# Kernel tuning notes

Measured on AMD Instinct MI355X. Metric: run time of the kernel, lower is better.

## Reference

```python
import jax, jax.numpy as jnp
import numpy as np

EPS = 1e-6
SCAL = 5.0
PARTS = 16
NFEAT = 32
RES = 64


def conv(x, w, b, stride=1):
    y = jax.lax.conv_general_dilated(x, w, (stride, stride), 'SAME',
                                     dimension_numbers=('NCHW', 'OIHW', 'NCHW'))
    return y + b[None, :, None, None]


def spatial_softmax(x):
    b, k, h, w = x.shape
    return jax.nn.softmax(x.reshape(b, k, h * w), axis=-1).reshape(b, k, h, w)


def make_grid(h, w):
    ys = jnp.linspace(-1.0, 1.0, h)
    xs = jnp.linspace(-1.0, 1.0, w)
    gy, gx = jnp.meshgrid(ys, xs, indexing='ij')
    return jnp.stack([gy, gx], axis=-1)  # [h, w, 2]


def e_sigma(x, w1, b1, w2, b2, wp, bp):
    # shared shape/appearance encoder: parts via spatial softmax + residual sum map
    h1 = jax.nn.relu(conv(x, w1, b1, stride=2))   # [B,64,64,64]
    h2 = jax.nn.relu(conv(h1, w2, b2))            # [B,64,64,64]
    parts = spatial_softmax(conv(h2, wp, bp))     # [B,16,64,64]
    return parts, h2


def e_alpha(x, w1, b1, w2, b2):
    h1 = jax.nn.relu(conv(x, w1, b1))
    return conv(h1, w2, b2)                       # [B,32,64,64]


def get_mu_and_prec(parts):
    # soft-argmax mean + 2x2 covariance -> inverse Cholesky factor L_inv
    b, k, h, w = parts.shape
    grid = make_grid(h, w)
    mu = jnp.einsum('bkhw,hwc->bkc', parts, grid)                       # [b,k,2]
    outer = jnp.einsum('hwm,hwn->hwmn', grid, grid)
    cov = jnp.einsum('bkhw,hwmn->bkmn', parts, outer) - jnp.einsum('bkm,bkn->bkmn', mu, mu)
    a = jnp.sqrt(cov[..., 0, 0] + EPS)
    bb = cov[..., 0, 1] / (a + EPS)
    c = jnp.sqrt(jnp.maximum(cov[..., 1, 1] - bb * bb, 0.0) + EPS)
    det = a * c
    z = jnp.zeros_like(a)
    L_inv = SCAL / (det[..., None, None] + EPS) * jnp.stack(
        [jnp.stack([c, z], axis=-1), jnp.stack([-bb, a], axis=-1)], axis=-2)  # [b,k,2,2]
    return mu, L_inv


def feat_mu_to_enc(alpha, mu, L_inv, h, w):
    # render Cauchy-shaped part heatmaps from (mu, L_inv) and paint part features
    grid = make_grid(h, w)
    dist = grid[None, None] - mu[:, :, None, None, :]        # [b,k,h,w,2]
    proj = jnp.einsum('bkhwi,bkij->bkhwj', dist, L_inv)
    heat = 1.0 / (1.0 + jnp.sum(proj * proj, axis=-1))       # [b,k,h,w]
    norm = heat / (jnp.sum(heat, axis=(2, 3), keepdims=True) + EPS)
    fmap = jnp.einsum('bkf,bkhw->bfhw', alpha, norm)         # [b,nf,h,w]
    return jnp.concatenate([heat, fmap], axis=1)             # [b,nk+nf,h,w]


def decoder(enc, w1, b1, w2, b2, w3, b3):
    h1 = jax.nn.relu(conv(enc, w1, b1))                      # [B,64,64,64]
    up = jnp.repeat(jnp.repeat(h1, 2, axis=2), 2, axis=3)    # nearest upsample -> 128
    h2 = jax.nn.relu(conv(up, w2, b2))
    return jax.nn.sigmoid(conv(h2, w3, b3))                  # [B,3,128,128]


def setup_inputs():
    key = jax.random.key(0)
    ks = jax.random.split(key, 16)
    def w(k, shape):
        fan_in = shape[1] * shape[2] * shape[3]
        return (jax.random.normal(k, shape, jnp.float32) / np.sqrt(fan_in)).astype(jnp.float32)
    B = 32
    return {
        'x': jax.random.uniform(ks[0], (B, 3, 128, 128), jnp.float32),
        'x_spatial_transform': jax.random.uniform(ks[1], (B, 3, 128, 128), jnp.float32),
        'x_appearance_transform': jax.random.uniform(ks[2], (B, 3, 128, 128), jnp.float32),
        'coord': jax.random.normal(ks[3], (B, PARTS, 2), jnp.float32) * 0.5,
        'vector': jax.random.normal(ks[4], (B, PARTS, 2), jnp.float32) * 0.1,
        'es_w1': w(ks[5], (RES, 3, 3, 3)), 'es_b1': jnp.zeros((RES,), jnp.float32),
        'es_w2': w(ks[6], (RES, RES, 3, 3)), 'es_b2': jnp.zeros((RES,), jnp.float32),
        'es_wp': w(ks[7], (PARTS, RES, 3, 3)), 'es_bp': jnp.zeros((PARTS,), jnp.float32),
        'ea_w1': w(ks[8], (RES, RES, 3, 3)), 'ea_b1': jnp.zeros((RES,), jnp.float32),
        'ea_w2': w(ks[9], (NFEAT, RES, 3, 3)), 'ea_b2': jnp.zeros((NFEAT,), jnp.float32),
        'd_w1': w(ks[10], (RES, PARTS + NFEAT, 3, 3)), 'd_b1': jnp.zeros((RES,), jnp.float32),
        'd_w2': w(ks[11], (32, RES, 3, 3)), 'd_b2': jnp.zeros((32,), jnp.float32),
        'd_w3': w(ks[12], (3, 32, 3, 3)), 'd_b3': jnp.zeros((3,), jnp.float32),
    }


def reference(x, x_spatial_transform, x_appearance_transform, coord, vector,
              es_w1, es_b1, es_w2, es_b2, es_wp, es_bp,
              ea_w1, ea_b1, ea_w2, ea_b2,
              d_w1, d_b1, d_w2, d_b2, d_w3, d_b3):
    # shape stream (appearance-transformed image -> geometry)
    shape_parts, _ = e_sigma(x_appearance_transform, es_w1, es_b1, es_w2, es_b2, es_wp, es_bp)
    mu, L_inv = get_mu_and_prec(shape_parts)
    # appearance stream (spatially-transformed image -> appearance)
    app_parts, app_sum = e_sigma(x_spatial_transform, es_w1, es_b1, es_w2, es_b2, es_wp, es_bp)
    f_xs = e_alpha(app_sum, ea_w1, ea_b1, ea_w2, ea_b2)
    # local part appearances: gather features under each part map
    alpha = jnp.einsum('bfhw,bkhw->bkf', f_xs, app_parts)
    encoding = feat_mu_to_enc(alpha, mu, L_inv, 64, 64)
    reconstruction = decoder(encoding, d_w1, d_b1, d_w2, d_b2, d_w3, d_b3)
    # composite loss
    mu_a, L_inv_a = get_mu_and_prec(app_parts)
    rec_loss = jnp.mean((x - reconstruction) ** 2)
    equiv_loss = jnp.mean((mu - mu_a) ** 2) + 0.01 * jnp.mean((L_inv - L_inv_a) ** 2)
    transport_loss = jnp.mean((mu_a - (coord + vector)) ** 2)
    loss = rec_loss + equiv_loss + transport_loss
    return reconstruction, loss
```

## Files before the change

kernel.cpp:

```cpp
#include <hip/hip_runtime.h>
#include <hip/hip_bf16.h>

#define EPS 1e-6f
#define SCAL 5.0f

typedef __attribute__((ext_vector_type(8))) short bf8v;
typedef __attribute__((ext_vector_type(4))) float f32x4;

#define OFF_MU     0
#define OFF_LINV   1024
#define OFF_MUA    3072
#define OFF_LINVA  4096
#define OFF_HSUM   6144
#define OFF_ALPHA  6656
#define OFF_REC    23040
#define OFF_R1     32768
#define OFF_R2     (OFF_R1 + 8388608)
#define OFF_R3     (OFF_R2 + 8388608)
#define WS_TOTAL   (OFF_R3 + 16777216)

#define BA_XA   ((size_t)2 * OFF_R3)
#define BA_X2   ((size_t)2 * OFF_R1)
#define OFF_PARTSF OFF_R2
#define OFF_PROBS  (OFF_R2 + 4194304)
#define BA_EA1  ((size_t)2 * OFF_R3)
#define OFF_FXS (OFF_R3 + 4194304)
#define BA_E    ((size_t)2 * OFF_R2)
#define BA_D1   ((size_t)2 * OFF_R1)
#define BA_D2   ((size_t)2 * OFF_R3)

#define WT_ESW1 0
#define WT_ESB1 1728
#define WT_ESB2 1792
#define WT_ESBP 1856
#define WT_EAB1 1872
#define WT_EAB2 1936
#define WT_DB1  1968
#define WT_DB2  2032
#define WT_W3P  2064
#define WT_DB3  2928
#define P_WP2  0
#define P_WPP  36864
#define P_WPA1 46080
#define P_WPA2 82944
#define P_WPD1 101376
#define P_WPD2 138240

__device__ __attribute__((aligned(16))) float g_ws[WS_TOTAL];
__device__ __attribute__((aligned(16))) float g_wt[3072];
__device__ __attribute__((aligned(16))) __hip_bfloat16 g_wp[156672];
__device__ int g_isbf16;

__device__ __forceinline__ float selz(bool c, float v) { return c ? v : 0.f; }
__device__ __forceinline__ float cvtbf(short s) {
    return __uint_as_float(((unsigned int)(unsigned short)s) << 16);
}
__device__ __forceinline__ short f2bf(float f) {
    unsigned u = __float_as_uint(f);
    u += 0x7fff + ((u >> 16) & 1);
    return (short)(u >> 16);
}
__device__ __forceinline__ float ldin(const void* p, size_t i, int bf) {
    return bf ? __bfloat162float(((const __hip_bfloat16*)p)[i])
              : ((const float*)p)[i];
}

__device__ __forceinline__ float block_sum(float v) {
    __shared__ float sb[8];
    for (int off = 32; off; off >>= 1) v += __shfl_down(v, off, 64);
    int lane = threadIdx.x & 63, wid = threadIdx.x >> 6;
    __syncthreads();
    if (lane == 0) sb[wid] = v;
    __syncthreads();
    float r = 0.f;
    for (int i = 0; i < 4; ++i) r += sb[i];
    return r;
}
__device__ __forceinline__ float block_max(float v) {
    __shared__ float sb[8];
    for (int off = 32; off; off >>= 1) v = fmaxf(v, __shfl_down(v, off, 64));
    int lane = threadIdx.x & 63, wid = threadIdx.x >> 6;
    __syncthreads();
    if (lane == 0) sb[wid] = v;
    __syncthreads();
    float r = -1e30f;
    for (int i = 0; i < 4; ++i) r = fmaxf(r, sb[i]);
    return r;
}

__global__ void detect_k(const void* x) {
    const __hip_bfloat16* p = (const __hip_bfloat16*)x;
    int lane = threadIdx.x & 63;
    float v = 0.f;
    for (int i = lane; i < 256; i += 64) {
        float a = fabsf(__bfloat162float(p[i]));
        if (!(a <= 2.0f)) v = 1.f;
    }
    for (int off = 32; off; off >>= 1) v += __shfl_down(v, off, 64);
    if (lane == 0) {
        g_isbf16 = (v == 0.f) ? 1 : 0;
        g_ws[OFF_REC] = 0.f;
    }
}

__global__ void wpack_k(const void* esw1, const void* esb1, const void* esw2, const void* esb2,
                        const void* eswp, const void* esbp, const void* eaw1, const void* eab1,
                        const void* eaw2, const void* eab2, const void* dw1, const void* db1,
                        const void* dw2, const void* db2, const void* dw3, const void* db3) {
    int bf = g_isbf16;
    int gid0 = blockIdx.x * 256 + threadIdx.x, stride = gridDim.x * 256;
    for (int g = gid0; g < 512; g += stride) g_ws[OFF_HSUM + g] = 0.f;
    for (int g = gid0; g < 1728; g += stride) g_wt[WT_ESW1 + g] = ldin(esw1, g, bf);
    for (int g = gid0; g < 64; g += stride) g_wt[WT_ESB1 + g] = ldin(esb1, g, bf);
    for (int g = gid0; g < 64; g += stride) g_wt[WT_ESB2 + g] = ldin(esb2, g, bf);
    for (int g = gid0; g < 16; g += stride) g_wt[WT_ESBP + g] = ldin(esbp, g, bf);
    for (int g = gid0; g < 64; g += stride) g_wt[WT_EAB1 + g] = ldin(eab1, g, bf);
    for (int g = gid0; g < 32; g += stride) g_wt[WT_EAB2 + g] = ldin(eab2, g, bf);
    for (int g = gid0; g < 64; g += stride) g_wt[WT_DB1 + g] = ldin(db1, g, bf);
    for (int g = gid0; g < 32; g += stride) g_wt[WT_DB2 + g] = ldin(db2, g, bf);
    for (int g = gid0; g < 3; g += stride) g_wt[WT_DB3 + g] = ldin(db3, g, bf);
    for (int g = gid0; g < 864; g += stride) {
        int t = g / 96, o = (g / 32) % 3, k = g & 31;
        g_wt[WT_W3P + g] = ldin(dw3, (size_t)(o * 32 + k) * 9 + t, bf);
    }
    for (int g = gid0; g < 36864; g += stride) {
        int t = g >> 12, n = (g >> 6) & 63, k = g & 63;
        g_wp[P_WP2 + g] = __float2bfloat16(ldin(esw2, (size_t)(n * 64 + k) * 9 + t, bf));
    }
    for (int g = gid0; g < 9216; g += stride) {
        int t = g >> 10, n = (g >> 6) & 15, k = g & 63;
        g_wp[P_WPP + g] = __float2bfloat16(ldin(eswp, (size_t)(n * 64 + k) * 9 + t, bf));
    }
    for (int g = gid0; g < 36864; g += stride) {
        int t = g >> 12, n = (g >> 6) & 63, k = g & 63;
        g_wp[P_WPA1 + g] = __float2bfloat16(ldin(eaw1, (size_t)(n * 64 + k) * 9 + t, bf));
    }
    for (int g = gid0; g < 18432; g += stride) {
        int t = g >> 11, n = (g >> 6) & 31, k = g & 63;
        g_wp[P_WPA2 + g] = __float2bfloat16(ldin(eaw2, (size_t)(n * 64 + k) * 9 + t, bf));
    }
    for (int g = gid0; g < 36864; g += stride) {
        int t = g >> 12, n = (g >> 6) & 63, k = g & 63;
        float v = (k < 48) ? ldin(dw1, (size_t)(n * 48 + k) * 9 + t, bf) : 0.f;
        g_wp[P_WPD1 + g] = __float2bfloat16(v);
    }
    for (int g = gid0; g < 18432; g += stride) {
        int t = g >> 11, n = (g >> 6) & 31, k = g & 63;
        g_wp[P_WPD2 + g] = __float2bfloat16(ldin(dw2, (size_t)(n * 64 + k) * 9 + t, bf));
    }
}

__global__ void __launch_bounds__(256)
conv_s2n_k(const void* __restrict__ inA, const void* __restrict__ inB) {
    int bf = g_isbf16;
    int tile = blockIdx.x & 15;
    int gb = blockIdx.x >> 4;
    int g = gb & 3, b = gb >> 2;
    const void* in = (b < 32) ? inA : inB;
    int bb = b & 31;
    int pix = tile * 256 + threadIdx.x;
    int y = pix >> 6, x = pix & 63;
    size_t inb = (size_t)bb * 3 * 16384;
    const float* W = g_wt + WT_ESW1 + (size_t)(g * 16) * 27;
    float acc[16];
    #pragma unroll
    for (int o = 0; o < 16; ++o) acc[o] = g_wt[WT_ESB1 + g * 16 + o];
    int iy0 = 2 * y, ix0 = 2 * x;
    bool my2 = (iy0 + 2 < 128), mx2 = (ix0 + 2 < 128);
    int iy2 = my2 ? iy0 + 2 : 127, ix2 = mx2 ? ix0 + 2 : 127;
    for (int ic = 0; ic < 3; ++ic) {
        size_t pb = inb + ic * 16384;
        float t[9];
        t[0] = ldin(in, pb + iy0 * 128 + ix0, bf);
        t[1] = ldin(in, pb + iy0 * 128 + ix0 + 1, bf);
        t[2] = selz(mx2, ldin(in, pb + iy0 * 128 + ix2, bf));
        t[3] = ldin(in, pb + (iy0 + 1) * 128 + ix0, bf);
        t[4] = ldin(in, pb + (iy0 + 1) * 128 + ix0 + 1, bf);
        t[5] = selz(mx2, ldin(in, pb + (iy0 + 1) * 128 + ix2, bf));
        t[6] = selz(my2, ldin(in, pb + iy2 * 128 + ix0, bf));
        t[7] = selz(my2, ldin(in, pb + iy2 * 128 + ix0 + 1, bf));
        t[8] = selz(my2 && mx2, ldin(in, pb + iy2 * 128 + ix2, bf));
        #pragma unroll
        for (int o = 0; o < 16; ++o) {
            const float* wr = W + (o * 3 + ic) * 9;
            float a = acc[o];
            #pragma unroll
            for (int j = 0; j < 9; ++j) a = fmaf(t[j], wr[j], a);
            acc[o] = a;
        }
    }
    __hip_bfloat16* out = (__hip_bfloat16*)g_ws + BA_XA + ((size_t)b * 4096 + pix) * 64 + g * 16;
    #pragma unroll
    for (int o = 0; o < 16; ++o) out[o] = __float2bfloat16(fmaxf(acc[o], 0.f));
}

template<int TR>
__device__ __forceinline__ void stage_tile(__hip_bfloat16* sA,
                                           const __hip_bfloat16* __restrict__ inb, int y0) {
    for (int g = threadIdx.x; g < TR * 512; g += 256) {
        int r = g >> 9;
        int rem = g & 511;
        int px = rem >> 3, j = rem & 7;
        int yy = y0 - 1 + r;
        int P = px + 1;
        bf8v v = (bf8v){0, 0, 0, 0, 0, 0, 0, 0};
        if (yy >= 0 && yy <= 63)
            v = *(const bf8v*)(inb + ((size_t)(yy * 64 + px) * 64 + j * 8));
        *(bf8v*)(sA + ((r * 66 + P) * 64 + ((j ^ (P & 7)) * 8))) = v;
    }
    if (threadIdx.x < TR * 16) {
        int g = threadIdx.x;
        int r = g >> 4, rem = g & 15, side = rem >> 3, j = rem & 7;
        int P = side ? 65 : 0;
        *(bf8v*)(sA + ((r * 66 + P) * 64 + ((j ^ (P & 7)) * 8))) = (bf8v){0, 0, 0, 0, 0, 0, 0, 0};
    }
}

template<int MS>
__device__ __forceinline__ void ld_a(const __hip_bfloat16* sA, int it, int rowIn,
                                     int l15, int quad, bf8v (&a)[MS]) {
    const int t = it >> 1, c = it & 1;
    const int dy = t / 3 - 1, dx = t % 3 - 1;
    const int r = rowIn + 1 + dy;
    const int j = c * 4 + quad;
    #pragma unroll
    for (int ms = 0; ms < MS; ++ms) {
        int P = ms * 16 + l15 + dx + 1;
        a[ms] = *(const bf8v*)(sA + ((r * 66 + P) * 64 + ((j ^ (P & 7)) * 8)));
    }
}
template<int TOTN, int NS>
__device__ __forceinline__ void ld_b(int it, int l15, int quad, int wp_off, bf8v (&bv)[NS]) {
    const int t = it >> 1, c = it & 1;
    #pragma unroll
    for (int ns = 0; ns < NS; ++ns)
        bv[ns] = *(const bf8v*)(g_wp + wp_off +
                 ((size_t)(t * TOTN + ns * 16 + l15) * 64 + c * 32 + quad * 8));
}

template<int TOTN, int NS, int MS>
__device__ __forceinline__ void conv_body(const __hip_bfloat16* sA, int rowIn,
                                          int l15, int quad, int wp_off,
                                          f32x4 (&acc)[MS][NS]) {
    bf8v bq[3][NS];
    bf8v a[2][MS];
    ld_b<TOTN, NS>(0, l15, quad, wp_off, bq[0]);
    ld_b<TOTN, NS>(1, l15, quad, wp_off, bq[1]);
    ld_a<MS>(sA, 0, rowIn, l15, quad, a[0]);
    #pragma unroll
    for (int it = 0; it < 18; ++it) {
        if (it + 2 < 18) ld_b<TOTN, NS>(it + 2, l15, quad, wp_off, bq[(it + 2) % 3]);
        if (it + 1 < 18) ld_a<MS>(sA, it + 1, rowIn, l15, quad, a[(it + 1) & 1]);
        #pragma unroll
        for (int ns = 0; ns < NS; ++ns)
            #pragma unroll
            for (int ms = 0; ms < MS; ++ms)
                acc[ms][ns] = __builtin_amdgcn_mfma_f32_16x16x32_bf16(
                    a[it & 1][ms], bq[it % 3][ns], acc[ms][ns], 0, 0, 0);
    }
}

template<int TOTN, int NS, int OUTF32, int RELU>
__device__ __forceinline__ void epi_std(f32x4 (&acc)[4][NS], int bO, int y,
                                        int l15, int quad, int bias_off, size_t out_off) {
    #pragma unroll
    for (int ns = 0; ns < NS; ++ns) {
        float bias = g_wt[bias_off + ns * 16 + l15];
        #pragma unroll
        for (int ms = 0; ms < 4; ++ms) {
            #pragma unroll
            for (int r = 0; r < 4; ++r) {
                int pix = ms * 16 + quad * 4 + r;
                float v = acc[ms][ns][r] + bias;
                if (RELU) v = fmaxf(v, 0.f);
                size_t o = out_off + ((size_t)(bO * 4096 + y * 64 + pix)) * TOTN + ns * 16 + l15;
                if (OUTF32) g_ws[o] = v;
                else ((__hip_bfloat16*)g_ws)[o] = __float2bfloat16(v);
            }
        }
    }
}

template<int TOTN, int NS, int OUTF32, int RELU>
__global__ void __launch_bounds__(256) __attribute__((amdgpu_waves_per_eu(2, 3)))
conv_mfl_k(size_t in_off, int wp_off, int bias_off, size_t out_off) {
    __shared__ __hip_bfloat16 sA[6 * 66 * 64];
    int wid = threadIdx.x >> 6, lane = threadIdx.x & 63;
    int l15 = lane & 15, quad = lane >> 4;
    int b = blockIdx.x >> 4, y0 = (blockIdx.x & 15) * 4;
    const __hip_bfloat16* inb = (const __hip_bfloat16*)g_ws + in_off + (size_t)b * 4096 * 64;
    stage_tile<6>(sA, inb, y0);
    __syncthreads();
    f32x4 acc[4][NS];
    #pragma unroll
    for (int ms = 0; ms < 4; ++ms)
        #pragma unroll
        for (int ns = 0; ns < NS; ++ns) acc[ms][ns] = (f32x4){0.f, 0.f, 0.f, 0.f};
    conv_body<TOTN, NS, 4>(sA, wid, l15, quad, wp_off, acc);
    epi_std<TOTN, NS, OUTF32, RELU>(acc, b, y0 + wid, l15, quad, bias_off, out_off);
}

__global__ void __launch_bounds__(256) __attribute__((amdgpu_waves_per_eu(2, 3)))
conv_pea_k() {
    __shared__ __hip_bfloat16 sA[6 * 66 * 64];
    int wid = threadIdx.x >> 6, lane = threadIdx.x & 63;
    int l15 = lane & 15, quad = lane >> 4;
    int b = blockIdx.x >> 4, y0 = (blockIdx.x & 15) * 4;
    int y = y0 + wid;
    const __hip_bfloat16* inb = (const __hip_bfloat16*)g_ws + BA_X2 + (size_t)b * 4096 * 64;
    stage_tile<6>(sA, inb, y0);
    __syncthreads();
    f32x4 accP[4][1];
    #pragma unroll
    for (int ms = 0; ms < 4; ++ms) accP[ms][0] = (f32x4){0.f, 0.f, 0.f, 0.f};
    conv_body<16, 1, 4>(sA, wid, l15, quad, P_WPP, accP);
    epi_std<16, 1, 1, 0>(accP, b, y, l15, quad, WT_ESBP, (size_t)OFF_PARTSF);
    if (b >= 32) {
        f32x4 accE[4][4];
        #pragma unroll
        for (int ms = 0; ms < 4; ++ms)
            #pragma unroll
            for (int ns = 0; ns < 4; ++ns) accE[ms][ns] = (f32x4){0.f, 0.f, 0.f, 0.f};
        conv_body<64, 4, 4>(sA, wid, l15, quad, P_WPA1, accE);
        epi_std<64, 4, 0, 1>(accE, b - 32, y, l15, quad, WT_EAB1, BA_EA1);
    }
}

__global__ void __launch_bounds__(256) __attribute__((amdgpu_waves_per_eu(2, 3)))
conv_upmf2_k(size_t in_off, int wp_off, int bias_off, size_t out_off) {
    __shared__ __hip_bfloat16 sA[4 * 66 * 64];
    int wid = threadIdx.x >> 6, lane = threadIdx.x & 63;
    int l15 = lane & 15, quad = lane >> 4;
    int b = blockIdx.x >> 5, y0 = (blockIdx.x & 31) * 4;
    int ri0 = (y0 >> 1) - 1;
    const __hip_bfloat16* inb = (const __hip_bfloat16*)g_ws + in_off + (size_t)b * 4096 * 64;
    for (int g = threadIdx.x; g < 2048; g += 256) {
        int r = g >> 9;
        int rem = g & 511;
        int px = rem >> 3, j = rem & 7;
        int yi = ri0 + r;
        int P = px + 1;
        bf8v v = (bf8v){0, 0, 0, 0, 0, 0, 0, 0};
        if (yi >= 0 && yi <= 63)
            v = *(const bf8v*)(inb + ((size_t)(yi * 64 + px) * 64 + j * 8));
        *(bf8v*)(sA + ((r * 66 + P) * 64 + ((j ^ (P & 7)) * 8))) = v;
    }
    if (threadIdx.x < 64) {
        int g = threadIdx.x;
        int r = g >> 4, rem = g & 15, side = rem >> 3, j = rem & 7;
        int P = side ? 65 : 0;
        *(bf8v*)(sA + ((r * 66 + P) * 64 + ((j ^ (P & 7)) * 8))) = (bf8v){0, 0, 0, 0, 0, 0, 0, 0};
    }
    __syncthreads();
    int y = y0 + wid;
    f32x4 acc[8][2];
    #pragma unroll
    for (int ms = 0; ms < 8; ++ms)
        #pragma unroll
        for (int ns = 0; ns < 2; ++ns) acc[ms][ns] = (f32x4){0.f, 0.f, 0.f, 0.f};
    bf8v bq[3][2];
    ld_b<32, 2>(0, l15, quad, wp_off, bq[0]);
    ld_b<32, 2>(1, l15, quad, wp_off, bq[1]);
    #pragma unroll
    for (int it = 0; it < 18; ++it) {
        if (it + 2 < 18) ld_b<32, 2>(it + 2, l15, quad, wp_off, bq[(it + 2) % 3]);
        const int t = it >> 1, c = it & 1;
        const int dy = t / 3 - 1, dx = t % 3 - 1;
        int yy = y + dy;
        if (yy >= 0 && yy <= 127) {
            int r = (yy >> 1) - ri0;
            int j = c * 4 + quad;
            bf8v a[8];
            #pragma unroll
            for (int ms = 0; ms < 8; ++ms) {
                int xx = ms * 16 + l15 + dx;
                int P = (xx < 0) ? 0 : ((xx > 127) ? 65 : ((xx >> 1) + 1));
                a[ms] = *(const bf8v*)(sA + ((r * 66 + P) * 64 + ((j ^ (P & 7)) * 8)));
            }
            #pragma unroll
            for (int ns = 0; ns < 2; ++ns)
                #pragma unroll
                for (int ms = 0; ms < 8; ++ms)
                    acc[ms][ns] = __builtin_amdgcn_mfma_f32_16x16x32_bf16(a[ms], bq[it % 3][ns], acc[ms][ns], 0, 0, 0);
        }
    }
    #pragma unroll
    for (int ns = 0; ns < 2; ++ns) {
        float bias = g_wt[bias_off + ns * 16 + l15];
        #pragma unroll
        for (int ms = 0; ms < 8; ++ms) {
            #pragma unroll
            for (int r = 0; r < 4; ++r) {
                int pix = ms * 16 + quad * 4 + r;
                float v = fmaxf(acc[ms][ns][r] + bias, 0.f);
                size_t o = out_off + ((size_t)(b * 16384 + y * 128 + pix)) * 32 + ns * 16 + l15;
                ((__hip_bfloat16*)g_ws)[o] = __float2bfloat16(v);
            }
        }
    }
}

__global__ void sm_mom3_k() {
    int bk = blockIdx.x;
    int b = bk >> 4, k = bk & 15;
    int app = (b >= 32);
    const float* P = g_ws + OFF_PARTSF + (size_t)b * 4096 * 16 + k;
    float r[16];
    #pragma unroll
    for (int j = 0; j < 16; ++j) r[j] = P[(size_t)(threadIdx.x + j * 256) * 16];
    float m = r[0];
    #pragma unroll
    for (int j = 1; j < 16; ++j) m = fmaxf(m, r[j]);
    m = block_max(m);
    float s = 0.f;
    #pragma unroll
    for (int j = 0; j < 16; ++j) { r[j] = __expf(r[j] - m); s += r[j]; }
    s = block_sum(s);
    float inv = 1.0f / s;
    float sy = 0, sx = 0, syy = 0, sxy = 0, sxx = 0;
    #pragma unroll
    for (int j = 0; j < 16; ++j) {
        float pv = r[j] * inv;
        int i = threadIdx.x + j * 256;
        if (app) g_ws[OFF_PROBS + ((size_t)(b - 32) * 16 + k) * 4096 + i] = pv;
        float gy = -1.0f + (i >> 6) * (2.0f / 63.0f);
        float gx = -1.0f + (i & 63) * (2.0f / 63.0f);
        sy += pv * gy; sx += pv * gx;
        syy += pv * gy * gy; sxy += pv * gy * gx; sxx += pv * gx * gx;
    }
    sy = block_sum(sy); sx = block_sum(sx);
    syy = block_sum(syy); sxy = block_sum(sxy); sxx = block_sum(sxx);
    if (threadIdx.x == 0) {
        float c00 = syy - sy * sy, c01 = sxy - sy * sx, c11 = sxx - sx * sx;
        float a = sqrtf(fmaxf(c00 + EPS, 1e-12f));
        float bb = c01 / (a + EPS);
        float cc = sqrtf(fmaxf(c11 - bb * bb, 0.f) + EPS);
        float det = a * cc;
        float sc = SCAL / (det + EPS);
        int idx = app ? ((b - 32) * 16 + k) : (b * 16 + k);
        int mu_off = app ? OFF_MUA : OFF_MU;
        int linv_off = app ? OFF_LINVA : OFF_LINV;
        g_ws[mu_off + idx * 2 + 0] = sy;
        g_ws[mu_off + idx * 2 + 1] = sx;
        g_ws[linv_off + idx * 4 + 0] = cc * sc;
        g_ws[linv_off + idx * 4 + 1] = 0.f;
        g_ws[linv_off + idx * 4 + 2] = -bb * sc;
        g_ws[linv_off + idx * 4 + 3] = a * sc;
    }
}

__global__ void alpha2_k() {
    int b = blockIdx.x & 31, k = blockIdx.x >> 5;
    int bk = b * 16 + k;
    __shared__ float pl[4096];
    const float* pr = g_ws + OFF_PROBS + (size_t)bk * 4096;
    for (int i = threadIdx.x; i < 4096; i += 256) pl[i] = pr[i];
    __syncthreads();
    float acc[32];
    #pragma unroll
    for (int f = 0; f < 32; ++f) acc[f] = 0.f;
    for (int i = threadIdx.x; i < 4096; i += 256) {
        float pv = pl[i];
        const float* fp = g_ws + OFF_FXS + (size_t)(b * 4096 + i) * 32;
        #pragma unroll
        for (int f = 0; f < 32; ++f) acc[f] = fmaf(pv, fp[f], acc[f]);
    }
    __shared__ float sw[4][32];
    int lane = threadIdx.x & 63, wid = threadIdx.x >> 6;
    #pragma unroll
    for (int f = 0; f < 32; ++f)
        for (int off = 32; off; off >>= 1) acc[f] += __shfl_down(acc[f], off, 64);
    if (lane == 0) {
        #pragma unroll
        for (int f = 0; f < 32; ++f) sw[wid][f] = acc[f];
    }
    __syncthreads();
    if (threadIdx.x < 32)
        g_ws[OFF_ALPHA + bk * 32 + threadIdx.x] =
            sw[0][threadIdx.x] + sw[1][threadIdx.x] + sw[2][threadIdx.x] + sw[3][threadIdx.x];
}

__global__ void heat2_k() {
    int tile = blockIdx.x & 15, b = blockIdx.x >> 4;
    __shared__ float hs[16];
    if (threadIdx.x < 16) hs[threadIdx.x] = 0.f;
    __syncthreads();
    int pix = tile * 256 + threadIdx.x;
    float gy = -1.0f + (pix >> 6) * (2.0f / 63.0f);
    float gx = -1.0f + (pix & 63) * (2.0f / 63.0f);
    bf8v e0, e1;
    float hv[16];
    #pragma unroll
    for (int k = 0; k < 16; ++k) {
        int bk = b * 16 + k;
        float m0 = g_ws[OFF_MU + bk * 2], m1 = g_ws[OFF_MU + bk * 2 + 1];
        float L00 = g_ws[OFF_LINV + bk * 4 + 0], L10 = g_ws[OFF_LINV + bk * 4 + 2],
              L11 = g_ws[OFF_LINV + bk * 4 + 3];
        float d0 = gy - m0, d1 = gx - m1;
        float p0 = d0 * L00 + d1 * L10;
        float p1 = d1 * L11;
        float h = 1.0f / (1.0f + p0 * p0 + p1 * p1);
        hv[k] = h;
        short sbits = f2bf(h);
        if (k < 8) e0[k] = sbits; else e1[k - 8] = sbits;
    }
    __hip_bfloat16* E = (__hip_bfloat16*)g_ws + BA_E + (size_t)(b * 4096 + pix) * 64;
    *(bf8v*)E = e0;
    *(bf8v*)(E + 8) = e1;
    #pragma unroll
    for (int k = 0; k < 16; ++k) {
        float v = hv[k];
        for (int off = 32; off; off >>= 1) v += __shfl_down(v, off, 64);
        if ((threadIdx.x & 63) == 0) atomicAdd(&hs[k], v);
    }
    __syncthreads();
    if (threadIdx.x < 16)
        atomicAdd(&g_ws[OFF_HSUM + b * 16 + threadIdx.x], hs[threadIdx.x]);
}

__global__ void fmap2_k() {
    int tile = blockIdx.x & 15, b = blockIdx.x >> 4;
    __shared__ float coef[16][32];
    for (int i = threadIdx.x; i < 512; i += 256) {
        int k = i >> 5, f = i & 31;
        coef[k][f] = g_ws[OFF_ALPHA + (b * 16 + k) * 32 + f] /
                     (g_ws[OFF_HSUM + b * 16 + k] + EPS);
    }
    __syncthreads();
    int pix = tile * 256 + threadIdx.x;
    __hip_bfloat16* E = (__hip_bfloat16*)g_ws + BA_E + (size_t)(b * 4096 + pix) * 64;
    float h[16];
    #pragma unroll
    for (int k = 0; k < 16; ++k) h[k] = __bfloat162float(E[k]);
    #pragma unroll
    for (int f = 0; f < 32; ++f) {
        float a = 0.f;
        #pragma unroll
        for (int k = 0; k < 16; ++k) a = fmaf(h[k], coef[k][f], a);
        E[16 + f] = __float2bfloat16(a);
    }
    #pragma unroll
    for (int z = 48; z < 64; ++z) E[z] = __float2bfloat16(0.f);
}

__global__ void __launch_bounds__(256)
conv_sign_k(const void* __restrict__ ximg, void* __restrict__ outp) {
    int bf = g_isbf16;
    int tile = blockIdx.x & 63, b = blockIdx.x >> 6;
    int pix = tile * 256 + threadIdx.x;
    int y = pix >> 7, x = pix & 127;
    const short* D2 = (const short*)((const __hip_bfloat16*)g_ws + BA_D2 + (size_t)b * 16384 * 32);
    float acc[3];
    #pragma unroll
    for (int o = 0; o < 3; ++o) acc[o] = g_wt[WT_DB3 + o];
    #pragma unroll
    for (int t = 0; t < 9; ++t) {
        int dy = t / 3 - 1, dx = t % 3 - 1;
        int yy = y + dy, xx = x + dx;
        if (yy < 0 || yy > 127 || xx < 0 || xx > 127) continue;
        const short* sp = D2 + (size_t)(yy * 128 + xx) * 32;
        #pragma unroll
        for (int c = 0; c < 4; ++c) {
            bf8v v = *(const bf8v*)(sp + c * 8);
            #pragma unroll
            for (int j = 0; j < 8; ++j) {
                float av = cvtbf(v[j]);
                int k = c * 8 + j;
                acc[0] = fmaf(av, g_wt[WT_W3P + (t * 3 + 0) * 32 + k], acc[0]);
                acc[1] = fmaf(av, g_wt[WT_W3P + (t * 3 + 1) * 32 + k], acc[1]);
                acc[2] = fmaf(av, g_wt[WT_W3P + (t * 3 + 2) * 32 + k], acc[2]);
            }
        }
    }
    float es = 0.f;
    #pragma unroll
    for (int o = 0; o < 3; ++o) {
        float v = 1.0f / (1.0f + __expf(-acc[o]));
        size_t oidx = ((size_t)b * 3 + o) * 16384 + pix;
        if (bf) ((__hip_bfloat16*)outp)[oidx] = __float2bfloat16(v);
        else    ((float*)outp)[oidx] = v;
        float e = ldin(ximg, oidx, bf) - v;
        es += e * e;
    }
    float s = block_sum(es);
    if (threadIdx.x == 0) atomicAdd(&g_ws[OFF_REC], s);
}

__global__ void loss_k(const void* __restrict__ coord,
                       const void* __restrict__ vec,
                       void* __restrict__ outp) {
    int bf = g_isbf16;
    const float* mu = g_ws + OFF_MU;
    const float* linv = g_ws + OFF_LINV;
    const float* mu_a = g_ws + OFF_MUA;
    const float* linv_a = g_ws + OFF_LINVA;
    float s1 = 0, s2 = 0, s3 = 0;
    for (int i = threadIdx.x; i < 1024; i += 256) {
        float d = mu[i] - mu_a[i];
        s1 += d * d;
        float t = ldin(coord, i, bf) + ldin(vec, i, bf);
        float d3 = mu_a[i] - t;
        s3 += d3 * d3;
    }
    for (int i = threadIdx.x; i < 2048; i += 256) {
        float d = linv[i] - linv_a[i];
        s2 += d * d;
    }
    s1 = block_sum(s1);
    s2 = block_sum(s2);
    s3 = block_sum(s3);
    if (threadIdx.x == 0) {
        float loss = g_ws[OFF_REC] / 1572864.0f + s1 / 1024.0f + 0.01f * (s2 / 2048.0f)
                   + s3 / 1024.0f;
        if (bf) ((__hip_bfloat16*)outp)[1572864] = __float2bfloat16(loss);
        else    ((float*)outp)[1572864] = loss;
    }
}

extern "C" void kernel_launch(void* const* d_in, const int* in_sizes, int n_in,
                              void* d_out, int out_size, void* d_ws, size_t ws_size,
                              hipStream_t stream) {
    const void* x     = d_in[0];
    const void* x_st  = d_in[1];
    const void* x_at  = d_in[2];
    const void* coord = d_in[3];
    const void* vec   = d_in[4];

    dim3 blk(256);

    detect_k<<<1, 64, 0, stream>>>(x);
    wpack_k<<<64, blk, 0, stream>>>(
        d_in[5],  d_in[6],  d_in[7],  d_in[8],
        d_in[9],  d_in[10], d_in[11], d_in[12],
        d_in[13], d_in[14], d_in[15], d_in[16],
        d_in[17], d_in[18], d_in[19], d_in[20]);

    conv_s2n_k<<<64 * 4 * 16, blk, 0, stream>>>(x_at, x_st);
    conv_mfl_k<64, 4, 0, 1><<<1024, blk, 0, stream>>>(BA_XA, P_WP2, WT_ESB2, BA_X2);

    conv_pea_k<<<1024, blk, 0, stream>>>();
    sm_mom3_k<<<1024, blk, 0, stream>>>();

    conv_mfl_k<32, 2, 1, 0><<<512, blk, 0, stream>>>(BA_EA1, P_WPA2, WT_EAB2, (size_t)OFF_FXS);
    alpha2_k<<<512, blk, 0, stream>>>();

    heat2_k<<<512, blk, 0, stream>>>();
    fmap2_k<<<512, blk, 0, stream>>>();

    conv_mfl_k<64, 4, 0, 1><<<512, blk, 0, stream>>>(BA_E, P_WPD1, WT_DB1, BA_D1);
    conv_upmf2_k<<<1024, blk, 0, stream>>>(BA_D1, P_WPD2, WT_DB2, BA_D2);
    conv_sign_k<<<32 * 64, blk, 0, stream>>>(x, d_out);

    loss_k<<<1, blk, 0, stream>>>(coord, vec, d_out);
}
```

Baseline: 417.8 us.

## Split conv warp tiles into two rows by half the output channels

Reorganises the warp work split in the MFMA conv kernels. Each of the four waves now computes two output rows for half of the output channels, instead of one row for all channels. Each wave therefore loads only half the weight fragments from global memory, and each weight fragment is reused across two rows. The cost is twice as many shared-memory A-fragment reads per weight set, with a similar accumulator register count.

```diff
diff --git a/kernel.cpp b/kernel.cpp
--- a/kernel.cpp
+++ b/kernel.cpp
@@ -229,13 +229,30 @@
         a[ms] = *(const bf8v*)(sA + ((r * 66 + P) * 64 + ((j ^ (P & 7)) * 8)));
     }
 }
+template<int MS>
+__device__ __forceinline__ void ld_a2(const __hip_bfloat16* sA, int it, int rowbase,
+                                      int l15, int quad, bf8v (&a)[2][MS]) {
+    const int t = it >> 1, c = it & 1;
+    const int dy = t / 3 - 1, dx = t % 3 - 1;
+    const int j = c * 4 + quad;
+    #pragma unroll
+    for (int rp = 0; rp < 2; ++rp) {
+        const int r = rowbase + rp + 1 + dy;
+        #pragma unroll
+        for (int ms = 0; ms < MS; ++ms) {
+            int P = ms * 16 + l15 + dx + 1;
+            a[rp][ms] = *(const bf8v*)(sA + ((r * 66 + P) * 64 + ((j ^ (P & 7)) * 8)));
+        }
+    }
+}
 template<int TOTN, int NS>
-__device__ __forceinline__ void ld_b(int it, int l15, int quad, int wp_off, bf8v (&bv)[NS]) {
+__device__ __forceinline__ void ld_b(int it, int ocoff, int l15, int quad, int wp_off,
+                                     bf8v (&bv)[NS]) {
     const int t = it >> 1, c = it & 1;
     #pragma unroll
     for (int ns = 0; ns < NS; ++ns)
         bv[ns] = *(const bf8v*)(g_wp + wp_off +
-                 ((size_t)(t * TOTN + ns * 16 + l15) * 64 + c * 32 + quad * 8));
+                 ((size_t)(t * TOTN + ocoff + ns * 16 + l15) * 64 + c * 32 + quad * 8));
 }
 
 template<int TOTN, int NS, int MS>
@@ -244,12 +261,12 @@
                                           f32x4 (&acc)[MS][NS]) {
     bf8v bq[3][NS];
     bf8v a[2][MS];
-    ld_b<TOTN, NS>(0, l15, quad, wp_off, bq[0]);
-    ld_b<TOTN, NS>(1, l15, quad, wp_off, bq[1]);
+    ld_b<TOTN, NS>(0, 0, l15, quad, wp_off, bq[0]);
+    ld_b<TOTN, NS>(1, 0, l15, quad, wp_off, bq[1]);
     ld_a<MS>(sA, 0, rowIn, l15, quad, a[0]);
     #pragma unroll
     for (int it = 0; it < 18; ++it) {
-        if (it + 2 < 18) ld_b<TOTN, NS>(it + 2, l15, quad, wp_off, bq[(it + 2) % 3]);
+        if (it + 2 < 18) ld_b<TOTN, NS>(it + 2, 0, l15, quad, wp_off, bq[(it + 2) % 3]);
         if (it + 1 < 18) ld_a<MS>(sA, it + 1, rowIn, l15, quad, a[(it + 1) & 1]);
         #pragma unroll
         for (int ns = 0; ns < NS; ++ns)
@@ -257,6 +274,30 @@
             for (int ms = 0; ms < MS; ++ms)
                 acc[ms][ns] = __builtin_amdgcn_mfma_f32_16x16x32_bf16(
                     a[it & 1][ms], bq[it % 3][ns], acc[ms][ns], 0, 0, 0);
+    }
+}
+
+template<int TOTN, int NSW, int MS>
+__device__ __forceinline__ void conv_body2(const __hip_bfloat16* sA, int rowbase, int ocoff,
+                                           int l15, int quad, int wp_off,
+                                           f32x4 (&acc)[2][MS][NSW]) {
+    bf8v bq[3][NSW];
+    bf8v a[2][2][MS];
+    ld_b<TOTN, NSW>(0, ocoff, l15, quad, wp_off, bq[0]);
+    ld_b<TOTN, NSW>(1, ocoff, l15, quad, wp_off, bq[1]);
+    ld_a2<MS>(sA, 0, rowbase, l15, quad, a[0]);
+    #pragma unroll
+    for (int it = 0; it < 18; ++it) {
+        if (it + 2 < 18) ld_b<TOTN, NSW>(it + 2, ocoff, l15, quad, wp_off, bq[(it + 2) % 3]);
+        if (it + 1 < 18) ld_a2<MS>(sA, it + 1, rowbase, l15, quad, a[(it + 1) & 1]);
+        #pragma unroll
+        for (int rp = 0; rp < 2; ++rp)
+            #pragma unroll
+            for (int ns = 0; ns < NSW; ++ns)
+                #pragma unroll
+                for (int ms = 0; ms < MS; ++ms)
+                    acc[rp][ms][ns] = __builtin_amdgcn_mfma_f32_16x16x32_bf16(
+                        a[it & 1][rp][ms], bq[it % 3][ns], acc[rp][ms][ns], 0, 0, 0);
     }
 }
 
@@ -280,24 +321,54 @@
         }
     }
 }
-
-template<int TOTN, int NS, int OUTF32, int RELU>
+template<int TOTN, int NSW, int OUTF32, int RELU>
+__device__ __forceinline__ void epi_2r(f32x4 (&acc)[2][4][NSW], int bO, int y0, int rowbase,
+                                       int ocoff, int l15, int quad, int bias_off,
+                                       size_t out_off) {
+    #pragma unroll
+    for (int rp = 0; rp < 2; ++rp) {
+        int y = y0 + rowbase + rp;
+        #pragma unroll
+        for (int ns = 0; ns < NSW; ++ns) {
+            float bias = g_wt[bias_off + ocoff + ns * 16 + l15];
+            #pragma unroll
+            for (int ms = 0; ms < 4; ++ms) {
+                #pragma unroll
+                for (int r = 0; r < 4; ++r) {
+                    int pix = ms * 16 + quad * 4 + r;
+                    float v = acc[rp][ms][ns][r] + bias;
+                    if (RELU) v = fmaxf(v, 0.f);
+                    size_t o = out_off + ((size_t)(bO * 4096 + y * 64 + pix)) * TOTN +
+                               ocoff + ns * 16 + l15;
+                    if (OUTF32) g_ws[o] = v;
+                    else ((__hip_bfloat16*)g_ws)[o] = __float2bfloat16(v);
+                }
+            }
+        }
+    }
+}
+
+template<int TOTN, int NSW, int OUTF32, int RELU>
 __global__ void __launch_bounds__(256) __attribute__((amdgpu_waves_per_eu(2, 3)))
 conv_mfl_k(size_t in_off, int wp_off, int bias_off, size_t out_off) {
     __shared__ __hip_bfloat16 sA[6 * 66 * 64];
     int wid = threadIdx.x >> 6, lane = threadIdx.x & 63;
     int l15 = lane & 15, quad = lane >> 4;
     int b = blockIdx.x >> 4, y0 = (blockIdx.x & 15) * 4;
+    int og = wid & 1, rowbase = (wid >> 1) * 2;
+    int ocoff = og * NSW * 16;
     const __hip_bfloat16* inb = (const __hip_bfloat16*)g_ws + in_off + (size_t)b * 4096 * 64;
     stage_tile<6>(sA, inb, y0);
     __syncthreads();
-    f32x4 acc[4][NS];
-    #pragma unroll
-    for (int ms = 0; ms < 4; ++ms)
-        #pragma unroll
-        for (int ns = 0; ns < NS; ++ns) acc[ms][ns] = (f32x4){0.f, 0.f, 0.f, 0.f};
-    conv_body<TOTN, NS, 4>(sA, wid, l15, quad, wp_off, acc);
-    epi_std<TOTN, NS, OUTF32, RELU>(acc, b, y0 + wid, l15, quad, bias_off, out_off);
+    f32x4 acc[2][4][NSW];
+    #pragma unroll
+    for (int rp = 0; rp < 2; ++rp)
+        #pragma unroll
+        for (int ms = 0; ms < 4; ++ms)
+            #pragma unroll
+            for (int ns = 0; ns < NSW; ++ns) acc[rp][ms][ns] = (f32x4){0.f, 0.f, 0.f, 0.f};
+    conv_body2<TOTN, NSW, 4>(sA, rowbase, ocoff, l15, quad, wp_off, acc);
+    epi_2r<TOTN, NSW, OUTF32, RELU>(acc, b, y0, rowbase, ocoff, l15, quad, bias_off, out_off);
 }
 
 __global__ void __launch_bounds__(256) __attribute__((amdgpu_waves_per_eu(2, 3)))
@@ -316,13 +387,17 @@
     conv_body<16, 1, 4>(sA, wid, l15, quad, P_WPP, accP);
     epi_std<16, 1, 1, 0>(accP, b, y, l15, quad, WT_ESBP, (size_t)OFF_PARTSF);
     if (b >= 32) {
-        f32x4 accE[4][4];
-        #pragma unroll
-        for (int ms = 0; ms < 4; ++ms)
-            #pragma unroll
-            for (int ns = 0; ns < 4; ++ns) accE[ms][ns] = (f32x4){0.f, 0.f, 0.f, 0.f};
-        conv_body<64, 4, 4>(sA, wid, l15, quad, P_WPA1, accE);
-        epi_std<64, 4, 0, 1>(accE, b - 32, y, l15, quad, WT_EAB1, BA_EA1);
+        int og = wid & 1, rowbase = (wid >> 1) * 2;
+        int ocoff = og * 32;
+        f32x4 accE[2][4][2];
+        #pragma unroll
+        for (int rp = 0; rp < 2; ++rp)
+            #pragma unroll
+            for (int ms = 0; ms < 4; ++ms)
+                #pragma unroll
+                for (int ns = 0; ns < 2; ++ns) accE[rp][ms][ns] = (f32x4){0.f, 0.f, 0.f, 0.f};
+        conv_body2<64, 2, 4>(sA, rowbase, ocoff, l15, quad, P_WPA1, accE);
+        epi_2r<64, 2, 0, 1>(accE, b - 32, y0, rowbase, ocoff, l15, quad, WT_EAB1, BA_EA1);
     }
 }
 
@@ -352,48 +427,50 @@
         *(bf8v*)(sA + ((r * 66 + P) * 64 + ((j ^ (P & 7)) * 8))) = (bf8v){0, 0, 0, 0, 0, 0, 0, 0};
     }
     __syncthreads();
-    int y = y0 + wid;
-    f32x4 acc[8][2];
-    #pragma unroll
-    for (int ms = 0; ms < 8; ++ms)
-        #pragma unroll
-        for (int ns = 0; ns < 2; ++ns) acc[ms][ns] = (f32x4){0.f, 0.f, 0.f, 0.f};
-    bf8v bq[3][2];
-    ld_b<32, 2>(0, l15, quad, wp_off, bq[0]);
-    ld_b<32, 2>(1, l15, quad, wp_off, bq[1]);
+    int og = wid & 1, rowbase = (wid >> 1) * 2;
+    f32x4 acc[2][8];
+    #pragma unroll
+    for (int rp = 0; rp < 2; ++rp)
+        #pragma unroll
+        for (int ms = 0; ms < 8; ++ms) acc[rp][ms] = (f32x4){0.f, 0.f, 0.f, 0.f};
+    bf8v bq[3][1];
+    ld_b<32, 1>(0, og * 16, l15, quad, wp_off, bq[0]);
+    ld_b<32, 1>(1, og * 16, l15, quad, wp_off, bq[1]);
     #pragma unroll
     for (int it = 0; it < 18; ++it) {
-        if (it + 2 < 18) ld_b<32, 2>(it + 2, l15, quad, wp_off, bq[(it + 2) % 3]);
+        if (it + 2 < 18) ld_b<32, 1>(it + 2, og * 16, l15, quad, wp_off, bq[(it + 2) % 3]);
         const int t = it >> 1, c = it & 1;
         const int dy = t / 3 - 1, dx = t % 3 - 1;
-        int yy = y + dy;
-        if (yy >= 0 && yy <= 127) {
-            int r = (yy >> 1) - ri0;
-            int j = c * 4 + quad;
-            bf8v a[8];
-            #pragma unroll
-            for (int ms = 0; ms < 8; ++ms) {
-                int xx = ms * 16 + l15 + dx;
-                int P = (xx < 0) ? 0 : ((xx > 127) ? 65 : ((xx >> 1) + 1));
-                a[ms] = *(const bf8v*)(sA + ((r * 66 + P) * 64 + ((j ^ (P & 7)) * 8)));
-            }
-            #pragma unroll
-            for (int ns = 0; ns < 2; ++ns)
+        #pragma unroll
+        for (int rp = 0; rp < 2; ++rp) {
+            int yy = y0 + rowbase + rp + dy;
+            if (yy >= 0 && yy <= 127) {
+                int r = (yy >> 1) - ri0;
+                int j = c * 4 + quad;
+                bf8v a[8];
+                #pragma unroll
+                for (int ms = 0; ms < 8; ++ms) {
+                    int xx = ms * 16 + l15 + dx;
+                    int P = (xx < 0) ? 0 : ((xx > 127) ? 65 : ((xx >> 1) + 1));
+                    a[ms] = *(const bf8v*)(sA + ((r * 66 + P) * 64 + ((j ^ (P & 7)) * 8)));
+                }
                 #pragma unroll
                 for (int ms = 0; ms < 8; ++ms)
-                    acc[ms][ns] = __builtin_amdgcn_mfma_f32_16x16x32_bf16(a[ms], bq[it % 3][ns], acc[ms][ns], 0, 0, 0);
+                    acc[rp][ms] = __builtin_amdgcn_mfma_f32_16x16x32_bf16(a[ms], bq[it % 3][0], acc[rp][ms], 0, 0, 0);
+            }
         }
     }
-    #pragma unroll
-    for (int ns = 0; ns < 2; ++ns) {
-        float bias = g_wt[bias_off + ns * 16 + l15];
+    float bias = g_wt[bias_off + og * 16 + l15];
+    #pragma unroll
+    for (int rp = 0; rp < 2; ++rp) {
+        int y = y0 + rowbase + rp;
         #pragma unroll
         for (int ms = 0; ms < 8; ++ms) {
             #pragma unroll
             for (int r = 0; r < 4; ++r) {
                 int pix = ms * 16 + quad * 4 + r;
-                float v = fmaxf(acc[ms][ns][r] + bias, 0.f);
-                size_t o = out_off + ((size_t)(b * 16384 + y * 128 + pix)) * 32 + ns * 16 + l15;
+                float v = fmaxf(acc[rp][ms][r] + bias, 0.f);
+                size_t o = out_off + ((size_t)(b * 16384 + y * 128 + pix)) * 32 + og * 16 + l15;
                 ((__hip_bfloat16*)g_ws)[o] = __float2bfloat16(v);
             }
         }
@@ -636,18 +713,18 @@
         d_in[17], d_in[18], d_in[19], d_in[20]);
 
     conv_s2n_k<<<64 * 4 * 16, blk, 0, stream>>>(x_at, x_st);
-    conv_mfl_k<64, 4, 0, 1><<<1024, blk, 0, stream>>>(BA_XA, P_WP2, WT_ESB2, BA_X2);
+    conv_mfl_k<64, 2, 0, 1><<<1024, blk, 0, stream>>>(BA_XA, P_WP2, WT_ESB2, BA_X2);
 
     conv_pea_k<<<1024, blk, 0, stream>>>();
     sm_mom3_k<<<1024, blk, 0, stream>>>();
 
-    conv_mfl_k<32, 2, 1, 0><<<512, blk, 0, stream>>>(BA_EA1, P_WPA2, WT_EAB2, (size_t)OFF_FXS);
+    conv_mfl_k<32, 1, 1, 0><<<512, blk, 0, stream>>>(BA_EA1, P_WPA2, WT_EAB2, (size_t)OFF_FXS);
     alpha2_k<<<512, blk, 0, stream>>>();
 
     heat2_k<<<512, blk, 0, stream>>>();
     fmap2_k<<<512, blk, 0, stream>>>();
 
-    conv_mfl_k<64, 4, 0, 1><<<512, blk, 0, stream>>>(BA_E, P_WPD1, WT_DB1, BA_D1);
+    conv_mfl_k<64, 2, 0, 1><<<512, blk, 0, stream>>>(BA_E, P_WPD1, WT_DB1, BA_D1);
     conv_upmf2_k<<<1024, blk, 0, stream>>>(BA_D1, P_WPD2, WT_DB2, BA_D2);
     conv_sign_k<<<32 * 64, blk, 0, stream>>>(x, d_out);
 
```

New measurement: 403.9 us. 1.03x faster.
